# Kernel optimization log

Measured on AMD Instinct MI355X. Metric: run time of the kernel, lower is better.

The kernel has to match this reference:

```python
import jax, jax.numpy as jnp
import numpy as np

HIDDEN = 51
LW = LH = 7


def setup_inputs() -> dict:
    key = jax.random.key(0)
    ks = jax.random.split(key, 14)
    N, T = 256, 2000
    s = lambda k, shape, fan_in: jax.random.uniform(k, shape, jnp.float32, -1.0, 1.0) / np.sqrt(fan_in)
    inp = {
        "stimulus": jax.random.normal(ks[0], (N, T, LH, LW), jnp.float32),
        # linear_layer: Linear(49 -> 1)
        "Wl": s(ks[1], (1, LW * LH), LW * LH),
        "bl": s(ks[2], (1,), LW * LH),
        # first_lstm: LSTMCell(1 -> 51)
        "Wih1": s(ks[3], (4 * HIDDEN, 1), HIDDEN),
        "Whh1": s(ks[4], (4 * HIDDEN, HIDDEN), HIDDEN),
        "bih1": s(ks[5], (4 * HIDDEN,), HIDDEN),
        "bhh1": s(ks[6], (4 * HIDDEN,), HIDDEN),
        # second_lstm: LSTMCell(51 -> 1)
        "Wih2": s(ks[7], (4 * 1, HIDDEN), 1),
        "Whh2": s(ks[8], (4 * 1, 1), 1),
        "bih2": s(ks[9], (4 * 1,), 1),
        "bhh2": s(ks[10], (4 * 1,), 1),
        # adjust_layer: Linear(1 -> 1)
        "Wa": s(ks[11], (1, 1), 1),
        "ba": s(ks[12], (1,), 1),
    }
    return inp


def _lstm_cell(x, h, c, Wih, Whh, bih, bhh):
    # PyTorch LSTMCell: gates order i, f, g, o
    gates = x @ Wih.T + bih + h @ Whh.T + bhh
    i, f, g, o = jnp.split(gates, 4, axis=-1)
    i = jax.nn.sigmoid(i)
    f = jax.nn.sigmoid(f)
    g = jnp.tanh(g)
    o = jax.nn.sigmoid(o)
    c_new = f * c + i * g
    h_new = o * jnp.tanh(c_new)
    return h_new, c_new


def reference(stimulus, Wl, bl, Wih1, Whh1, bih1, bhh1, Wih2, Whh2, bih2, bhh2, Wa, ba):
    N, T = stimulus.shape[0], stimulus.shape[1]
    x = stimulus.reshape(N, T, LW * LH)
    # Time-independent input projection + ReLU, done once for all steps: (N, T, 1)
    x_lin = jax.nn.relu(jnp.einsum("ntf,of->nto", x, Wl) + bl)

    h1_0 = jnp.zeros((N, HIDDEN), stimulus.dtype)
    c1_0 = jnp.zeros((N, HIDDEN), stimulus.dtype)
    h2_0 = jnp.zeros((N, 1), stimulus.dtype)
    c2_0 = jnp.zeros((N, 1), stimulus.dtype)

    def step(carry, xt):
        h1, c1, h2, c2 = carry
        h1, c1 = _lstm_cell(xt, h1, c1, Wih1, Whh1, bih1, bhh1)
        h2, c2 = _lstm_cell(h1, h2, c2, Wih2, Whh2, bih2, bhh2)
        out = h2 @ Wa.T + ba  # (N, 1)
        return (h1, c1, h2, c2), out[:, 0]

    xs = jnp.swapaxes(x_lin, 0, 1)  # (T, N, 1)
    _, outs = jax.lax.scan(step, (h1_0, c1_0, h2_0, c2_0), xs)
    return jnp.swapaxes(outs, 0, 1)  # (N, T)
```

## Files before the change

### kernel.cpp

```cpp
#include <hip/hip_runtime.h>

#define T_STEPS 2000
#define NBATCH  256
#define HID     51
#define FEAT    49
#define ROWF4   784
#define XTOT4   (NBATCH * T_STEPS * FEAT / 4)
#define PSTRIDE 5

typedef _Float16 v2h __attribute__((ext_vector_type(2)));

__device__ __forceinline__ float rl(float v, int lane) {
    return __int_as_float(__builtin_amdgcn_readlane(__float_as_int(v), lane));
}
__device__ __forceinline__ int rli(int v, int lane) {
    return __builtin_amdgcn_readlane(v, lane);
}
__device__ __forceinline__ float sigmoidf_fast(float x) {
    return __builtin_amdgcn_rcpf(1.0f + __builtin_amdgcn_exp2f(-1.4426950408889634f * x));
}
__device__ __forceinline__ float tanhf_fast(float x) {
    return 1.0f - 2.0f * __builtin_amdgcn_rcpf(1.0f + __builtin_amdgcn_exp2f(2.8853900817779268f * x));
}
__device__ __forceinline__ int packh2(float lo, float hi) {
    v2h p = (v2h){(_Float16)lo, (_Float16)hi};
    return __builtin_bit_cast(int, p);
}
__device__ __forceinline__ float dot2(int w, int h, float acc) {
    return __builtin_amdgcn_fdot2(__builtin_bit_cast(v2h, w),
                                  __builtin_bit_cast(v2h, h), acc, false);
}
__device__ __forceinline__ void bar_lds() {
    asm volatile("s_waitcnt lgkmcnt(0)" ::: "memory");
    __builtin_amdgcn_s_barrier();
    asm volatile("" ::: "memory");
}
__device__ __forceinline__ float row_dot(const float* row, const float* __restrict__ Wl) {
    float a0 = 0, a1 = 0, a2 = 0, a3 = 0, a4 = 0, a5 = 0, a6 = 0;
#pragma unroll
    for (int j = 0; j < FEAT; j += 7) {
        a0 = fmaf(row[j    ], Wl[j    ], a0);
        a1 = fmaf(row[j + 1], Wl[j + 1], a1);
        a2 = fmaf(row[j + 2], Wl[j + 2], a2);
        a3 = fmaf(row[j + 3], Wl[j + 3], a3);
        a4 = fmaf(row[j + 4], Wl[j + 4], a4);
        a5 = fmaf(row[j + 5], Wl[j + 5], a5);
        a6 = fmaf(row[j + 6], Wl[j + 6], a6);
    }
    return ((a0 + a1) + (a2 + a3)) + ((a4 + a5) + a6);
}

#define REP26(F) F(0) F(1) F(2) F(3) F(4) F(5) F(6) F(7) F(8) F(9) F(10) F(11) F(12) \
                 F(13) F(14) F(15) F(16) F(17) F(18) F(19) F(20) F(21) F(22) F(23) F(24) F(25)

__global__ __attribute__((amdgpu_flat_work_group_size(256, 256), amdgpu_waves_per_eu(1)))
void rnn_kernel(
    const float* __restrict__ x,
    const float* __restrict__ Wl, const float* __restrict__ bl,
    const float* __restrict__ Wih1, const float* __restrict__ Whh1,
    const float* __restrict__ bih1, const float* __restrict__ bhh1,
    const float* __restrict__ Wih2, const float* __restrict__ Whh2,
    const float* __restrict__ bih2, const float* __restrict__ bhh2,
    const float* __restrict__ Wa, const float* __restrict__ ba,
    float* __restrict__ out)
{
    const int n    = blockIdx.x;
    const int tid  = threadIdx.x;
    const int wid  = tid >> 6;
    const int lane = tid & 63;
    float* optr = out + (size_t)n * T_STEPS;
    const float4* x4 = (const float4*)x;
    const int sbase = n * (T_STEPS * FEAT / 4);

    __shared__ float xt_[64 * FEAT];
    __shared__ float pt[2][64 * PSTRIDE];
    __shared__ float ob[64];
    float4* t4 = (float4*)xt_;

#define DECLW(j) int w_##j; int sh_##j;
    REP26(DECLW)
    {
        const float* srow;
        float msk;
        if (lane < HID) { srow = Whh1 + (wid * HID + lane) * HID; msk = 1.0f; }
        else            { srow = Wih2 + wid * HID; msk = (lane == HID) ? 1.0f : 0.0f; }
        const float wh2 = Whh2[wid] * ((lane == HID) ? 1.0f : 0.0f);
#define LOADW(j) { \
        float lo = srow[2*(j)] * msk; \
        float hi = (2*(j)+1 < HID) ? srow[2*(j)+1] * msk : wh2; \
        w_##j = packh2(lo, hi); \
        asm("" : "+v"(w_##j)); }
        REP26(LOADW)
    }

    float wx = 0.0f, b = 0.0f;
    if (lane < HID) {
        wx = Wih1[wid * HID + lane];
        b  = bih1[wid * HID + lane] + bhh1[wid * HID + lane];
    } else if (lane == HID) {
        b  = bih2[wid] + bhh2[wid];
    }
    const float wav = Wa[0], bav = ba[0];
    const float bl0 = bl[0];

#define INITS(j) sh_##j = 0;
    REP26(INITS)

    float c = 0.0f, h = 0.0f;

    float4 p0, p1, p2, p3;
#define PF(base) { \
        int g0_ = (base) + tid;       g0_ = g0_ < XTOT4 ? g0_ : (XTOT4 - 1); p0 = x4[g0_]; \
        int g1_ = (base) + 256 + tid; g1_ = g1_ < XTOT4 ? g1_ : (XTOT4 - 1); p1 = x4[g1_]; \
        int g2_ = (base) + 512 + tid; g2_ = g2_ < XTOT4 ? g2_ : (XTOT4 - 1); p2 = x4[g2_]; \
        if (tid < 16) { int g3_ = (base) + 768 + tid; g3_ = g3_ < XTOT4 ? g3_ : (XTOT4 - 1); p3 = x4[g3_]; } }
#define COMMIT { t4[tid] = p0; t4[tid + 256] = p1; t4[tid + 512] = p2; \
                 if (tid < 16) t4[tid + 768] = p3; }
#define ROWDOT(dst) { float d_ = row_dot(&xt_[lane * FEAT], Wl); \
                      dst = fmaxf(d_ + bl0, 0.0f); }

    float xa, xb;
    PF(sbase)              COMMIT  bar_lds();  ROWDOT(xa)
    PF(sbase + ROWF4)      bar_lds();  COMMIT  bar_lds();  ROWDOT(xb)
    PF(sbase + 2 * ROWF4)

    const int prow = lane * PSTRIDE;

#pragma unroll 1
    for (int t = 0; t <= T_STEPS; ++t) {
        if ((t & 63) == 0 && t > 0 && t < T_STEPS) {
            const int k = t >> 6;
            if (wid == 0) {
                int oi = 64 * (k - 1) - 1 + lane;
                float ov = ob[lane];
                if (oi >= 0) optr[oi] = ov;
            }
            xa = xb;
            COMMIT
            bar_lds();
            ROWDOT(xb)
            PF(sbase + (k + 2) * ROWF4)
        }
        float xt = rl(xa, t & 63);

        float aA = fmaf(wx, xt, b), aB = 0.0f;
#define DOT(j) { if ((j) & 1) aB = dot2(w_##j, sh_##j, aB); \
                 else         aA = dot2(w_##j, sh_##j, aA); }
        REP26(DOT)
        float a = aA + aB;

        float act = (wid == 2) ? tanhf_fast(a) : sigmoidf_fast(a);

        float* ptw = pt[t & 1];
        ptw[prow + wid] = act;
        bar_lds();
        float ig = ptw[prow + 0];
        float fg = ptw[prow + 1];
        float gg = ptw[prow + 2];
        float og = ptw[prow + 3];

        c = fmaf(fg, c, ig * gg);
        h = og * tanhf_fast(c);
        if (t == 0 && lane >= HID) { c = 0.0f; h = 0.0f; }

        if (wid == 0 && lane == HID && t > 0)
            ob[t & 63] = fmaf(h, wav, bav);

        int hz = (int)(unsigned)__builtin_bit_cast(unsigned short, (_Float16)h);
        int nb = __builtin_amdgcn_mov_dpp(hz, 0xB1, 0xF, 0xF, true);
        int pair = hz | (nb << 16);
#define BCAST(j) sh_##j = rli(pair, 2 * (j));
        REP26(BCAST)
    }

    if (wid == 0 && lane <= 16) optr[1983 + lane] = ob[lane];
}

extern "C" void kernel_launch(void* const* d_in, const int* in_sizes, int n_in,
                              void* d_out, int out_size, void* d_ws, size_t ws_size,
                              hipStream_t stream) {
    const float* x    = (const float*)d_in[0];
    const float* Wl   = (const float*)d_in[1];
    const float* bl   = (const float*)d_in[2];
    const float* Wih1 = (const float*)d_in[3];
    const float* Whh1 = (const float*)d_in[4];
    const float* bih1 = (const float*)d_in[5];
    const float* bhh1 = (const float*)d_in[6];
    const float* Wih2 = (const float*)d_in[7];
    const float* Whh2 = (const float*)d_in[8];
    const float* bih2 = (const float*)d_in[9];
    const float* bhh2 = (const float*)d_in[10];
    const float* Wa   = (const float*)d_in[11];
    const float* ba   = (const float*)d_in[12];
    float* out = (float*)d_out;

    rnn_kernel<<<NBATCH, 256, 0, stream>>>(x, Wl, bl, Wih1, Whh1, bih1, bhh1,
                                           Wih2, Whh2, bih2, bhh2, Wa, ba, out);
}
```

Before: 871.8 us.

## Collapse four gate waves into one wave per sequence, removing per-step barriers

Each block now runs a single 64-lane wave that holds all four gate weight rows in registers and computes i, f, g, o locally. This removes the per-step LDS exchange of gate activations and the workgroup barrier on every timestep, along with the barriers around staging the input tiles. In exchange each step does four times the dot2 work in one wave, so register pressure rises sharply (104 packed weight registers plus 13 float4 prefetch buffers). Only 256 waves run in total, so machine parallelism drops.

```diff
diff --git a/kernel.cpp b/kernel.cpp
--- a/kernel.cpp
+++ b/kernel.cpp
@@ -6,7 +6,6 @@
 #define FEAT    49
 #define ROWF4   784
 #define XTOT4   (NBATCH * T_STEPS * FEAT / 4)
-#define PSTRIDE 5
 
 typedef _Float16 v2h __attribute__((ext_vector_type(2)));
 
@@ -29,11 +28,6 @@
 __device__ __forceinline__ float dot2(int w, int h, float acc) {
     return __builtin_amdgcn_fdot2(__builtin_bit_cast(v2h, w),
                                   __builtin_bit_cast(v2h, h), acc, false);
-}
-__device__ __forceinline__ void bar_lds() {
-    asm volatile("s_waitcnt lgkmcnt(0)" ::: "memory");
-    __builtin_amdgcn_s_barrier();
-    asm volatile("" ::: "memory");
 }
 __device__ __forceinline__ float row_dot(const float* row, const float* __restrict__ Wl) {
     float a0 = 0, a1 = 0, a2 = 0, a3 = 0, a4 = 0, a5 = 0, a6 = 0;
@@ -53,7 +47,7 @@
 #define REP26(F) F(0) F(1) F(2) F(3) F(4) F(5) F(6) F(7) F(8) F(9) F(10) F(11) F(12) \
                  F(13) F(14) F(15) F(16) F(17) F(18) F(19) F(20) F(21) F(22) F(23) F(24) F(25)
 
-__global__ __attribute__((amdgpu_flat_work_group_size(256, 256), amdgpu_waves_per_eu(1)))
+__global__ __attribute__((amdgpu_flat_work_group_size(64, 64), amdgpu_waves_per_eu(1)))
 void rnn_kernel(
     const float* __restrict__ x,
     const float* __restrict__ Wl, const float* __restrict__ bl,
@@ -65,40 +59,46 @@
     float* __restrict__ out)
 {
     const int n    = blockIdx.x;
-    const int tid  = threadIdx.x;
-    const int wid  = tid >> 6;
-    const int lane = tid & 63;
+    const int lane = threadIdx.x;
     float* optr = out + (size_t)n * T_STEPS;
     const float4* x4 = (const float4*)x;
     const int sbase = n * (T_STEPS * FEAT / 4);
 
     __shared__ float xt_[64 * FEAT];
-    __shared__ float pt[2][64 * PSTRIDE];
     __shared__ float ob[64];
     float4* t4 = (float4*)xt_;
 
-#define DECLW(j) int w_##j; int sh_##j;
+#define DECLW(j) int w0_##j, w1_##j, w2_##j, w3_##j; int sh_##j;
     REP26(DECLW)
-    {
-        const float* srow;
-        float msk;
-        if (lane < HID) { srow = Whh1 + (wid * HID + lane) * HID; msk = 1.0f; }
-        else            { srow = Wih2 + wid * HID; msk = (lane == HID) ? 1.0f : 0.0f; }
-        const float wh2 = Whh2[wid] * ((lane == HID) ? 1.0f : 0.0f);
-#define LOADW(j) { \
-        float lo = srow[2*(j)] * msk; \
+
+    const float msk = (lane <= HID) ? 1.0f : 0.0f;
+    const float m51 = (lane == HID) ? 1.0f : 0.0f;
+#define LOADW(j, wv) { float lo = srow[2*(j)] * msk; \
         float hi = (2*(j)+1 < HID) ? srow[2*(j)+1] * msk : wh2; \
-        w_##j = packh2(lo, hi); \
-        asm("" : "+v"(w_##j)); }
-        REP26(LOADW)
-    }
-
-    float wx = 0.0f, b = 0.0f;
+        wv##_##j = packh2(lo, hi); asm("" : "+v"(wv##_##j)); }
+#define LOADW0(j) LOADW(j, w0)
+#define LOADW1(j) LOADW(j, w1)
+#define LOADW2(j) LOADW(j, w2)
+#define LOADW3(j) LOADW(j, w3)
+    { const float* srow = (lane < HID) ? (Whh1 + (0 * HID + lane) * HID) : (Wih2 + 0 * HID);
+      const float wh2 = Whh2[0] * m51;  REP26(LOADW0) }
+    { const float* srow = (lane < HID) ? (Whh1 + (1 * HID + lane) * HID) : (Wih2 + 1 * HID);
+      const float wh2 = Whh2[1] * m51;  REP26(LOADW1) }
+    { const float* srow = (lane < HID) ? (Whh1 + (2 * HID + lane) * HID) : (Wih2 + 2 * HID);
+      const float wh2 = Whh2[2] * m51;  REP26(LOADW2) }
+    { const float* srow = (lane < HID) ? (Whh1 + (3 * HID + lane) * HID) : (Wih2 + 3 * HID);
+      const float wh2 = Whh2[3] * m51;  REP26(LOADW3) }
+
+    float wx0 = 0, wx1 = 0, wx2 = 0, wx3 = 0;
+    float b0 = 0, b1 = 0, b2 = 0, b3 = 0;
     if (lane < HID) {
-        wx = Wih1[wid * HID + lane];
-        b  = bih1[wid * HID + lane] + bhh1[wid * HID + lane];
+        wx0 = Wih1[0 * HID + lane]; b0 = bih1[0 * HID + lane] + bhh1[0 * HID + lane];
+        wx1 = Wih1[1 * HID + lane]; b1 = bih1[1 * HID + lane] + bhh1[1 * HID + lane];
+        wx2 = Wih1[2 * HID + lane]; b2 = bih1[2 * HID + lane] + bhh1[2 * HID + lane];
+        wx3 = Wih1[3 * HID + lane]; b3 = bih1[3 * HID + lane] + bhh1[3 * HID + lane];
     } else if (lane == HID) {
-        b  = bih2[wid] + bhh2[wid];
+        b0 = bih2[0] + bhh2[0]; b1 = bih2[1] + bhh2[1];
+        b2 = bih2[2] + bhh2[2]; b3 = bih2[3] + bhh2[3];
     }
     const float wav = Wa[0], bav = ba[0];
     const float bl0 = bl[0];
@@ -108,72 +108,76 @@
 
     float c = 0.0f, h = 0.0f;
 
-    float4 p0, p1, p2, p3;
-#define PF(base) { \
-        int g0_ = (base) + tid;       g0_ = g0_ < XTOT4 ? g0_ : (XTOT4 - 1); p0 = x4[g0_]; \
-        int g1_ = (base) + 256 + tid; g1_ = g1_ < XTOT4 ? g1_ : (XTOT4 - 1); p1 = x4[g1_]; \
-        int g2_ = (base) + 512 + tid; g2_ = g2_ < XTOT4 ? g2_ : (XTOT4 - 1); p2 = x4[g2_]; \
-        if (tid < 16) { int g3_ = (base) + 768 + tid; g3_ = g3_ < XTOT4 ? g3_ : (XTOT4 - 1); p3 = x4[g3_]; } }
-#define COMMIT { t4[tid] = p0; t4[tid + 256] = p1; t4[tid + 512] = p2; \
-                 if (tid < 16) t4[tid + 768] = p3; }
+    float4 pf0, pf1, pf2, pf3, pf4, pf5, pf6, pf7, pf8, pf9, pf10, pf11, pf12;
+#define PFALL(base) { int g_; \
+    g_=(base)+  0+lane; g_=g_<XTOT4?g_:(XTOT4-1); pf0 =x4[g_]; \
+    g_=(base)+ 64+lane; g_=g_<XTOT4?g_:(XTOT4-1); pf1 =x4[g_]; \
+    g_=(base)+128+lane; g_=g_<XTOT4?g_:(XTOT4-1); pf2 =x4[g_]; \
+    g_=(base)+192+lane; g_=g_<XTOT4?g_:(XTOT4-1); pf3 =x4[g_]; \
+    g_=(base)+256+lane; g_=g_<XTOT4?g_:(XTOT4-1); pf4 =x4[g_]; \
+    g_=(base)+320+lane; g_=g_<XTOT4?g_:(XTOT4-1); pf5 =x4[g_]; \
+    g_=(base)+384+lane; g_=g_<XTOT4?g_:(XTOT4-1); pf6 =x4[g_]; \
+    g_=(base)+448+lane; g_=g_<XTOT4?g_:(XTOT4-1); pf7 =x4[g_]; \
+    g_=(base)+512+lane; g_=g_<XTOT4?g_:(XTOT4-1); pf8 =x4[g_]; \
+    g_=(base)+576+lane; g_=g_<XTOT4?g_:(XTOT4-1); pf9 =x4[g_]; \
+    g_=(base)+640+lane; g_=g_<XTOT4?g_:(XTOT4-1); pf10=x4[g_]; \
+    g_=(base)+704+lane; g_=g_<XTOT4?g_:(XTOT4-1); pf11=x4[g_]; \
+    g_=(base)+768+lane; g_=g_<XTOT4?g_:(XTOT4-1); pf12=x4[g_]; }
+#define COMMIT { t4[  0+lane]=pf0;  t4[ 64+lane]=pf1;  t4[128+lane]=pf2; \
+                 t4[192+lane]=pf3;  t4[256+lane]=pf4;  t4[320+lane]=pf5; \
+                 t4[384+lane]=pf6;  t4[448+lane]=pf7;  t4[512+lane]=pf8; \
+                 t4[576+lane]=pf9;  t4[640+lane]=pf10; t4[704+lane]=pf11; \
+                 if (lane < 16) t4[768+lane]=pf12; }
 #define ROWDOT(dst) { float d_ = row_dot(&xt_[lane * FEAT], Wl); \
                       dst = fmaxf(d_ + bl0, 0.0f); }
 
     float xa, xb;
-    PF(sbase)              COMMIT  bar_lds();  ROWDOT(xa)
-    PF(sbase + ROWF4)      bar_lds();  COMMIT  bar_lds();  ROWDOT(xb)
-    PF(sbase + 2 * ROWF4)
-
-    const int prow = lane * PSTRIDE;
+    PFALL(sbase)              COMMIT  ROWDOT(xa)
+    PFALL(sbase + ROWF4)      COMMIT  ROWDOT(xb)
+    PFALL(sbase + 2 * ROWF4)
 
 #pragma unroll 1
     for (int t = 0; t <= T_STEPS; ++t) {
         if ((t & 63) == 0 && t > 0 && t < T_STEPS) {
             const int k = t >> 6;
-            if (wid == 0) {
-                int oi = 64 * (k - 1) - 1 + lane;
-                float ov = ob[lane];
-                if (oi >= 0) optr[oi] = ov;
-            }
             xa = xb;
             COMMIT
-            bar_lds();
             ROWDOT(xb)
-            PF(sbase + (k + 2) * ROWF4)
+            PFALL(sbase + (k + 2) * ROWF4)
         }
-        float xt = rl(xa, t & 63);
-
-        float aA = fmaf(wx, xt, b), aB = 0.0f;
-#define DOT(j) { if ((j) & 1) aB = dot2(w_##j, sh_##j, aB); \
-                 else         aA = dot2(w_##j, sh_##j, aA); }
+        const float xt = rl(xa, t & 63);
+
+        float a0A = fmaf(wx0, xt, b0), a0B = 0.0f;
+        float a1A = fmaf(wx1, xt, b1), a1B = 0.0f;
+        float a2A = fmaf(wx2, xt, b2), a2B = 0.0f;
+        float a3A = fmaf(wx3, xt, b3), a3B = 0.0f;
+#define DOT(j) { if ((j) & 1) { a0B = dot2(w0_##j, sh_##j, a0B); a1B = dot2(w1_##j, sh_##j, a1B); \
+                                a2B = dot2(w2_##j, sh_##j, a2B); a3B = dot2(w3_##j, sh_##j, a3B); } \
+                 else         { a0A = dot2(w0_##j, sh_##j, a0A); a1A = dot2(w1_##j, sh_##j, a1A); \
+                                a2A = dot2(w2_##j, sh_##j, a2A); a3A = dot2(w3_##j, sh_##j, a3A); } }
         REP26(DOT)
-        float a = aA + aB;
-
-        float act = (wid == 2) ? tanhf_fast(a) : sigmoidf_fast(a);
-
-        float* ptw = pt[t & 1];
-        ptw[prow + wid] = act;
-        bar_lds();
-        float ig = ptw[prow + 0];
-        float fg = ptw[prow + 1];
-        float gg = ptw[prow + 2];
-        float og = ptw[prow + 3];
-
-        c = fmaf(fg, c, ig * gg);
-        h = og * tanhf_fast(c);
+
+        const float gi = sigmoidf_fast(a0A + a0B);
+        const float gf = sigmoidf_fast(a1A + a1B);
+        const float gg = tanhf_fast(a2A + a2B);
+        const float go = sigmoidf_fast(a3A + a3B);
+
+        c = fmaf(gf, c, gi * gg);
+        h = go * tanhf_fast(c);
         if (t == 0 && lane >= HID) { c = 0.0f; h = 0.0f; }
 
-        if (wid == 0 && lane == HID && t > 0)
-            ob[t & 63] = fmaf(h, wav, bav);
+        if (lane == HID && t > 0) ob[(t - 1) & 63] = fmaf(h, wav, bav);
 
         int hz = (int)(unsigned)__builtin_bit_cast(unsigned short, (_Float16)h);
         int nb = __builtin_amdgcn_mov_dpp(hz, 0xB1, 0xF, 0xF, true);
         int pair = hz | (nb << 16);
 #define BCAST(j) sh_##j = rli(pair, 2 * (j));
         REP26(BCAST)
+
+        if ((t & 63) == 0 && t > 0) optr[t - 64 + lane] = ob[lane];
     }
 
-    if (wid == 0 && lane <= 16) optr[1983 + lane] = ob[lane];
+    if (lane < 16) optr[1984 + lane] = ob[lane];
 }
 
 extern "C" void kernel_launch(void* const* d_in, const int* in_sizes, int n_in,
@@ -194,6 +198,6 @@
     const float* ba   = (const float*)d_in[12];
     float* out = (float*)d_out;
 
-    rnn_kernel<<<NBATCH, 256, 0, stream>>>(x, Wl, bl, Wih1, Whh1, bih1, bhh1,
-                                           Wih2, Whh2, bih2, bhh2, Wa, ba, out);
-}
+    rnn_kernel<<<NBATCH, 64, 0, stream>>>(x, Wl, bl, Wih1, Whh1, bih1, bhh1,
+                                          Wih2, Whh2, bih2, bhh2, Wa, ba, out);
+}
```

Result: slower. 1.006 ms (+15.3%).
